# Optimization experiments

Measured on AMD Instinct MI355X. Metric: run time of the kernel, lower is better.

Reference implementation:

```python
import jax, jax.numpy as jnp
import numpy as np

N = 100_000   # nodes
E = 1_600_000 # edges (avg degree 16)
D = 64        # in_dim == hidden_dim


def setup_inputs() -> dict:
    key = jax.random.key(0)
    ks = jax.random.split(key, 9)
    scale = 1.0 / np.sqrt(D)
    x = jax.random.normal(ks[0], (N, D), jnp.float32)
    edge_index = jax.random.randint(ks[1], (2, E), 0, N, dtype=jnp.int32)
    W0 = jax.random.normal(ks[2], (D, D), jnp.float32) * scale
    b0 = jnp.zeros((D,), jnp.float32)
    W1 = jax.random.normal(ks[3], (D, D), jnp.float32) * scale
    b1 = jnp.zeros((D,), jnp.float32)
    W2 = jax.random.normal(ks[4], (D, D), jnp.float32) * scale
    b2 = jnp.zeros((D,), jnp.float32)
    return {"x": x, "edge_index": edge_index, "W0": W0, "b0": b0,
            "W1": W1, "b1": b1, "W2": W2, "b2": b2}


def _gcn_layer(h, W, b, src, dst, norm):
    # h: [N, D]; src/dst: [E+N] (self-loops included); norm: [E+N]
    h = h @ W                                  # dense transform [N, D]
    msg = h[src] * norm[:, None]               # gather + scale  [E+N, D]
    out = jax.ops.segment_sum(msg, dst, num_segments=N)  # scatter-add [N, D]
    return out + b


def reference(x, edge_index, W0, b0, W1, b1, W2, b2):
    loops = jnp.arange(N, dtype=edge_index.dtype)
    src = jnp.concatenate([edge_index[0], loops])  # [E+N]
    dst = jnp.concatenate([edge_index[1], loops])  # [E+N]
    # symmetric GCN normalization with self-loops (PyG gcn_norm)
    deg = jax.ops.segment_sum(jnp.ones_like(dst, dtype=x.dtype), dst, num_segments=N)
    d_inv = jnp.where(deg > 0, jax.lax.rsqrt(deg), 0.0)
    norm = d_inv[src] * d_inv[dst]                 # [E+N]
    for W, b in ((W0, b0), (W1, b1), (W2, b2)):
        x = jax.nn.relu(_gcn_layer(x, W, b, src, dst, norm))
    return x
```

## Files before the change

kernel.cpp:

```cpp
#include <hip/hip_runtime.h>
#include <hip/hip_fp16.h>


#define THREADS 256
#define BSH     9
#define BNODES  512
#define BCAP    9216
#define BPAD    16
#define CHUNK   4096

#if defined(__has_builtin)
#if __has_builtin(__builtin_amdgcn_fdot2) && __has_builtin(__builtin_amdgcn_perm)
#define USE_DOT2 1
#endif
#endif

typedef __attribute__((ext_vector_type(2))) _Float16 h2v;
typedef __attribute__((ext_vector_type(8))) _Float16 f16x8;
typedef __attribute__((ext_vector_type(4))) float    f32x4;

__global__ __launch_bounds__(THREADS)
void bin_kernel(const int* __restrict__ src, const int* __restrict__ dst,
                int* __restrict__ bcur, int* __restrict__ sbuf, int E) {
    __shared__ int cntb[THREADS];
    __shared__ int lstart[THREADS];
    __shared__ int gbase[THREADS];
    __shared__ int lcur[THREADS];
    __shared__ int tmp[THREADS];
    __shared__ int stagep[CHUNK];
    __shared__ unsigned char stageb[CHUNK];
    int tid = threadIdx.x;
    int e0  = blockIdx.x * CHUNK;
    int cnt = min(CHUNK, E - e0);
    int dreg[16];
#pragma unroll
    for (int j = 0; j < 16; ++j) {
        int i = tid + j * THREADS;
        dreg[j] = (i < cnt) ? dst[e0 + i] : -1;
    }
    cntb[tid] = 0;
    __syncthreads();
#pragma unroll
    for (int j = 0; j < 16; ++j)
        if (dreg[j] >= 0) atomicAdd(&cntb[dreg[j] >> BSH], 1);
    __syncthreads();
    int v = cntb[tid];
    tmp[tid] = v;
    __syncthreads();
    for (int off = 1; off < THREADS; off <<= 1) {
        int t = (tid >= off) ? tmp[tid - off] : 0;
        __syncthreads();
        tmp[tid] += t;
        __syncthreads();
    }
    lstart[tid] = tmp[tid] - v;
    lcur[tid]   = 0;
    if (v > 0) gbase[tid] = atomicAdd(&bcur[tid * BPAD], v);
    __syncthreads();
#pragma unroll
    for (int j = 0; j < 16; ++j) {
        int i = tid + j * THREADS;
        if (i < cnt) {
            int s = src[e0 + i];
            int d = dreg[j];
            int b = d >> BSH;
            int pos = atomicAdd(&lcur[b], 1);
            int idx = lstart[b] + pos;
            stagep[idx] = (s << BSH) | (d & (BNODES - 1));
            stageb[idx] = (unsigned char)b;
        }
    }
    __syncthreads();
    for (int i = tid; i < cnt; i += THREADS) {
        int b = stageb[i];
        sbuf[(size_t)b * BCAP + gbase[b] + (i - lstart[b])] = stagep[i];
    }
}

__global__ __launch_bounds__(THREADS)
void bscan_kernel(const int* __restrict__ bcur, int* __restrict__ bbase,
                  int NB, int* __restrict__ rowptr, int N, int E) {
    __shared__ int tmp[THREADS];
    int tid = threadIdx.x;
    int c = (tid < NB) ? min(bcur[tid * BPAD], BCAP) : 0;
    tmp[tid] = c;
    __syncthreads();
    for (int off = 1; off < THREADS; off <<= 1) {
        int t = (tid >= off) ? tmp[tid - off] : 0;
        __syncthreads();
        tmp[tid] += t;
        __syncthreads();
    }
    if (tid < NB) bbase[tid] = tmp[tid] - c;
    if (tid == 0) rowptr[N] = E;
}

__global__ __launch_bounds__(THREADS)
void finalize_kernel(const int* __restrict__ sbuf, const int* __restrict__ bcur,
                     const int* __restrict__ bbase, int* __restrict__ rowptr,
                     float* __restrict__ dinv, int* __restrict__ csrc, int N) {
    __shared__ int lcnt[BNODES];
    __shared__ int lexcl[BNODES];
    __shared__ int lcur[BNODES];
    __shared__ int tmp[THREADS];
    int b   = blockIdx.x;
    int tid = threadIdx.x;
    int cnt = min(bcur[b * BPAD], BCAP);
    int gb  = bbase[b];
    const int* sb = sbuf + (size_t)b * BCAP;
    for (int i = tid; i < BNODES; i += THREADS) { lcnt[i] = 0; lcur[i] = 0; }
    __syncthreads();
    for (int e = tid; e < cnt; e += THREADS)
        atomicAdd(&lcnt[sb[e] & (BNODES - 1)], 1);
    __syncthreads();
    int a0 = lcnt[2 * tid], a1 = lcnt[2 * tid + 1];
    int s  = a0 + a1;
    tmp[tid] = s;
    __syncthreads();
    for (int off = 1; off < THREADS; off <<= 1) {
        int t = (tid >= off) ? tmp[tid - off] : 0;
        __syncthreads();
        tmp[tid] += t;
        __syncthreads();
    }
    int ex = tmp[tid] - s;
    lexcl[2 * tid]     = ex;
    lexcl[2 * tid + 1] = ex + a0;
    int node = (b << BSH) + 2 * tid;
    if (node < N) {
        rowptr[node] = gb + ex;
        dinv[node]   = rsqrtf((float)(a0 + 1));
    }
    if (node + 1 < N) {
        rowptr[node + 1] = gb + ex + a0;
        dinv[node + 1]   = rsqrtf((float)(a1 + 1));
    }
    __syncthreads();
    for (int e = tid; e < cnt; e += THREADS) {
        int vv  = sb[e];
        int d   = vv & (BNODES - 1);
        int pos = atomicAdd(&lcur[d], 1);
        csrc[gb + lexcl[d] + pos] = vv >> BSH;
    }
}

__global__ __launch_bounds__(THREADS)
void gemm64_kernel(const float* __restrict__ X, __half* __restrict__ H,
                   const float* __restrict__ W, const float* __restrict__ dinv,
                   int n) {
    int lane = threadIdx.x & 63;
    int qk   = lane >> 4;
    int l16  = lane & 15;
    f16x8 bf[4][2];
#pragma unroll
    for (int t = 0; t < 4; ++t)
#pragma unroll
        for (int h = 0; h < 2; ++h) {
            const float* wp = W + (size_t)(32 * h + qk * 8) * 64 + 16 * t + l16;
#pragma unroll
            for (int j = 0; j < 8; ++j)
                bf[t][h][j] = (_Float16)wp[j * 64];
        }
    int wave  = (blockIdx.x * blockDim.x + threadIdx.x) >> 6;
    int nw    = (gridDim.x * blockDim.x) >> 6;
    int ntile = (n + 15) >> 4;
    for (int tile = wave; tile < ntile; tile += nw) {
        int rbase = tile << 4;
        int arow  = rbase + l16;
        if (arow >= n) arow = n - 1;
        const float4* xp = (const float4*)(X + (size_t)arow * 64 + qk * 8);
        float4 a0 = xp[0], a1 = xp[1];
        float4 a2 = xp[8], a3 = xp[9];
        f16x8 A0, A1;
        A0[0] = (_Float16)a0.x; A0[1] = (_Float16)a0.y;
        A0[2] = (_Float16)a0.z; A0[3] = (_Float16)a0.w;
        A0[4] = (_Float16)a1.x; A0[5] = (_Float16)a1.y;
        A0[6] = (_Float16)a1.z; A0[7] = (_Float16)a1.w;
        A1[0] = (_Float16)a2.x; A1[1] = (_Float16)a2.y;
        A1[2] = (_Float16)a2.z; A1[3] = (_Float16)a2.w;
        A1[4] = (_Float16)a3.x; A1[5] = (_Float16)a3.y;
        A1[6] = (_Float16)a3.z; A1[7] = (_Float16)a3.w;
        f32x4 acc[4];
#pragma unroll
        for (int t = 0; t < 4; ++t) {
            acc[t] = (f32x4){0.f, 0.f, 0.f, 0.f};
            acc[t] = __builtin_amdgcn_mfma_f32_16x16x32_f16(A0, bf[t][0], acc[t], 0, 0, 0);
            acc[t] = __builtin_amdgcn_mfma_f32_16x16x32_f16(A1, bf[t][1], acc[t], 0, 0, 0);
        }
        float dv[4];
#pragma unroll
        for (int r = 0; r < 4; ++r) {
            int row = rbase + qk * 4 + r;
            dv[r] = (row < n) ? dinv[row] : 0.f;
        }
#pragma unroll
        for (int r = 0; r < 4; ++r) {
            int row = rbase + qk * 4 + r;
            if (row < n) {
                __half* hp = H + (size_t)row * 64 + l16;
#pragma unroll
                for (int t = 0; t < 4; ++t)
                    hp[16 * t] = __float2half(acc[t][r] * dv[r]);
            }
        }
    }
}

__global__ __launch_bounds__(THREADS)
void agg_kernel(const __half* __restrict__ H, float* __restrict__ Y,
                const int* __restrict__ rowptr, const int* __restrict__ csrc,
                const float* __restrict__ dinv, const float* __restrict__ bias,
                int n) {
    int lane = threadIdx.x & 63;
    int grp  = lane >> 3;
    int sub  = lane & 7;
    int fl   = sub * 8;
    const int4* H4 = (const int4*)H;
    int wave = (blockIdx.x * blockDim.x + threadIdx.x) >> 6;
    int nw   = (gridDim.x * blockDim.x) >> 6;
    float4 bv0 = *(const float4*)(bias + fl);
    float4 bv1 = *(const float4*)(bias + fl + 4);
    for (int i = wave; i < n; i += nw) {
        int k0 = rowptr[i], k1 = rowptr[i + 1];
        float accf[8] = {0.f, 0.f, 0.f, 0.f, 0.f, 0.f, 0.f, 0.f};
        if (grp == 0) {
            int4 hv = H4[(size_t)i * 8 + sub];
            const __half2* hh = (const __half2*)&hv;
#pragma unroll
            for (int j = 0; j < 4; ++j) {
                float2 f = __half22float2(hh[j]);
                accf[2 * j]     += f.x;
                accf[2 * j + 1] += f.y;
            }
        }
        for (int basek = k0; basek < k1; basek += 16) {
            int kA = basek + grp, kB = kA + 8;
            bool vA = kA < k1, vB = kB < k1;
            int sA = vA ? csrc[kA] : 0;
            int sB = vB ? csrc[kB] : 0;
            int4 hA = H4[(size_t)sA * 8 + sub];
            int4 hB = H4[(size_t)sB * 8 + sub];
#ifdef USE_DOT2
            unsigned mb = (vA ? 0x3C00u : 0u) | (vB ? 0x3C000000u : 0u);
            h2v m2 = __builtin_bit_cast(h2v, mb);
            const unsigned* pa = (const unsigned*)&hA;
            const unsigned* pb = (const unsigned*)&hB;
#pragma unroll
            for (int j = 0; j < 4; ++j) {
                unsigned p0 = __builtin_amdgcn_perm(pb[j], pa[j], 0x05040100);
                unsigned p1 = __builtin_amdgcn_perm(pb[j], pa[j], 0x07060302);
                accf[2 * j]     = __builtin_amdgcn_fdot2(
                    __builtin_bit_cast(h2v, p0), m2, accf[2 * j], false);
                accf[2 * j + 1] = __builtin_amdgcn_fdot2(
                    __builtin_bit_cast(h2v, p1), m2, accf[2 * j + 1], false);
            }
#else
            float mA = vA ? 1.f : 0.f, mB = vB ? 1.f : 0.f;
            const __half2* ha = (const __half2*)&hA;
            const __half2* hb = (const __half2*)&hB;
#pragma unroll
            for (int j = 0; j < 4; ++j) {
                float2 fa = __half22float2(ha[j]);
                float2 fb = __half22float2(hb[j]);
                accf[2 * j]     = fmaf(fa.x, mA, accf[2 * j]);
                accf[2 * j]     = fmaf(fb.x, mB, accf[2 * j]);
                accf[2 * j + 1] = fmaf(fa.y, mA, accf[2 * j + 1]);
                accf[2 * j + 1] = fmaf(fb.y, mB, accf[2 * j + 1]);
            }
#endif
        }
#pragma unroll
        for (int j = 0; j < 8; ++j) {
            float a = accf[j];
            a += __shfl_xor(a, 8);
            a += __shfl_xor(a, 16);
            a += __shfl_xor(a, 32);
            accf[j] = a;
        }
        if (grp == 0) {
            float di = dinv[i];
            float4 o0, o1;
            o0.x = fmaxf(fmaf(accf[0], di, bv0.x), 0.f);
            o0.y = fmaxf(fmaf(accf[1], di, bv0.y), 0.f);
            o0.z = fmaxf(fmaf(accf[2], di, bv0.z), 0.f);
            o0.w = fmaxf(fmaf(accf[3], di, bv0.w), 0.f);
            o1.x = fmaxf(fmaf(accf[4], di, bv1.x), 0.f);
            o1.y = fmaxf(fmaf(accf[5], di, bv1.y), 0.f);
            o1.z = fmaxf(fmaf(accf[6], di, bv1.z), 0.f);
            o1.w = fmaxf(fmaf(accf[7], di, bv1.w), 0.f);
            *(float4*)(Y + (size_t)i * 64 + fl)     = o0;
            *(float4*)(Y + (size_t)i * 64 + fl + 4) = o1;
        }
    }
}

extern "C" void kernel_launch(void* const* d_in, const int* in_sizes, int n_in,
                              void* d_out, int out_size, void* d_ws, size_t ws_size,
                              hipStream_t stream) {
    const float* x  = (const float*)d_in[0];
    const int*   ei = (const int*)d_in[1];
    const float* W0 = (const float*)d_in[2];
    const float* b0 = (const float*)d_in[3];
    const float* W1 = (const float*)d_in[4];
    const float* b1 = (const float*)d_in[5];
    const float* W2 = (const float*)d_in[6];
    const float* b2 = (const float*)d_in[7];

    const int N = in_sizes[0] / 64;
    const int E = in_sizes[1] / 2;
    const int* src = ei;
    const int* dst = ei + E;
    const int NB = (N + BNODES - 1) >> BSH;

    char*  ws  = (char*)d_ws;
    size_t off = 0;
    auto alloc = [&](size_t bytes) -> void* {
        void* p = ws + off;
        off += (bytes + 255) & ~(size_t)255;
        return p;
    };
    int*    rowptr = (int*)   alloc((size_t)(N + 1) * 4);
    float*  dinv   = (float*) alloc((size_t)N * 4);
    int*    csrc   = (int*)   alloc((size_t)E * 4);
    int*    bcur   = (int*)   alloc((size_t)NB * BPAD * 4);
    int*    bbase  = (int*)   alloc((size_t)NB * 4);
    float*  actA   = (float*) alloc((size_t)N * 64 * 4);
    __half* hbuf   = (__half*)alloc((size_t)N * 64 * 2);
    int*    sbuf   = (int*)actA;
    float*  outb   = (float*)d_out;

    hipMemsetAsync(bcur, 0, (size_t)NB * BPAD * 4, stream);

    const int ngrid = 2048;
    const int ggrid = 1024;
    const int bgrid = (E + CHUNK - 1) / CHUNK;

    bin_kernel     <<<bgrid, THREADS, 0, stream>>>(src, dst, bcur, sbuf, E);
    bscan_kernel   <<<1,     THREADS, 0, stream>>>(bcur, bbase, NB, rowptr, N, E);
    finalize_kernel<<<NB,    THREADS, 0, stream>>>(sbuf, bcur, bbase, rowptr,
                                                   dinv, csrc, N);

    gemm64_kernel<<<ggrid, THREADS, 0, stream>>>(x, hbuf, W0, dinv, N);
    agg_kernel   <<<ngrid, THREADS, 0, stream>>>(hbuf, actA, rowptr, csrc, dinv, b0, N);
    gemm64_kernel<<<ggrid, THREADS, 0, stream>>>(actA, hbuf, W1, dinv, N);
    agg_kernel   <<<ngrid, THREADS, 0, stream>>>(hbuf, outb, rowptr, csrc, dinv, b1, N);
    gemm64_kernel<<<ggrid, THREADS, 0, stream>>>(outb, hbuf, W2, dinv, N);
    agg_kernel   <<<ngrid, THREADS, 0, stream>>>(hbuf, outb, rowptr, csrc, dinv, b2, N);
}
```

Measured before the change: 201.9 us.

## Process two nodes per wave in aggregation with prefetched row bounds

The aggregation kernel now splits each 64-lane wave into two 32-lane halves, each handling its own destination node. Each half loads four neighbor rows per iteration instead of two per 8-lane group, and the cross-lane reduction drops one shuffle stage. The next node's rowptr bounds are prefetched before the current node is processed, to hide that load latency. The intent is less lane idling for average degree around 17, which under-fills a 16-edge step per wave, in exchange for slightly more complex indexing. The GEMM epilogue also moves the dinv load inside the row guard.

Result: faster. 185.2 us (-8.2%).

```diff
diff --git a/kernel.cpp b/kernel.cpp
--- a/kernel.cpp
+++ b/kernel.cpp
@@ -187,23 +187,50 @@
             acc[t] = __builtin_amdgcn_mfma_f32_16x16x32_f16(A0, bf[t][0], acc[t], 0, 0, 0);
             acc[t] = __builtin_amdgcn_mfma_f32_16x16x32_f16(A1, bf[t][1], acc[t], 0, 0, 0);
         }
-        float dv[4];
-#pragma unroll
-        for (int r = 0; r < 4; ++r) {
-            int row = rbase + qk * 4 + r;
-            dv[r] = (row < n) ? dinv[row] : 0.f;
-        }
 #pragma unroll
         for (int r = 0; r < 4; ++r) {
             int row = rbase + qk * 4 + r;
             if (row < n) {
+                float dv = dinv[row];
                 __half* hp = H + (size_t)row * 64 + l16;
 #pragma unroll
                 for (int t = 0; t < 4; ++t)
-                    hp[16 * t] = __float2half(acc[t][r] * dv[r]);
+                    hp[16 * t] = __float2half(acc[t][r] * dv);
             }
         }
     }
+}
+
+__device__ __forceinline__ void pairdot(const int4& hA, const int4& hB,
+                                        bool vA, bool vB, float* accf) {
+#ifdef USE_DOT2
+    unsigned mb = (vA ? 0x3C00u : 0u) | (vB ? 0x3C000000u : 0u);
+    h2v m2 = __builtin_bit_cast(h2v, mb);
+    const unsigned* pa = (const unsigned*)&hA;
+    const unsigned* pb = (const unsigned*)&hB;
+#pragma unroll
+    for (int j = 0; j < 4; ++j) {
+        unsigned p0 = __builtin_amdgcn_perm(pb[j], pa[j], 0x05040100);
+        unsigned p1 = __builtin_amdgcn_perm(pb[j], pa[j], 0x07060302);
+        accf[2 * j]     = __builtin_amdgcn_fdot2(
+            __builtin_bit_cast(h2v, p0), m2, accf[2 * j], false);
+        accf[2 * j + 1] = __builtin_amdgcn_fdot2(
+            __builtin_bit_cast(h2v, p1), m2, accf[2 * j + 1], false);
+    }
+#else
+    float mA = vA ? 1.f : 0.f, mB = vB ? 1.f : 0.f;
+    const __half2* ha = (const __half2*)&hA;
+    const __half2* hb = (const __half2*)&hB;
+#pragma unroll
+    for (int j = 0; j < 4; ++j) {
+        float2 fa = __half22float2(ha[j]);
+        float2 fb = __half22float2(hb[j]);
+        accf[2 * j]     = fmaf(fa.x, mA, accf[2 * j]);
+        accf[2 * j]     = fmaf(fb.x, mB, accf[2 * j]);
+        accf[2 * j + 1] = fmaf(fa.y, mA, accf[2 * j + 1]);
+        accf[2 * j + 1] = fmaf(fb.y, mB, accf[2 * j + 1]);
+    }
+#endif
 }
 
 __global__ __launch_bounds__(THREADS)
@@ -212,73 +239,67 @@
                 const float* __restrict__ dinv, const float* __restrict__ bias,
                 int n) {
     int lane = threadIdx.x & 63;
-    int grp  = lane >> 3;
+    int half = lane >> 5;
+    int hl   = lane & 31;
+    int grp  = hl >> 3;
     int sub  = lane & 7;
     int fl   = sub * 8;
     const int4* H4 = (const int4*)H;
     int wave = (blockIdx.x * blockDim.x + threadIdx.x) >> 6;
     int nw   = (gridDim.x * blockDim.x) >> 6;
+    int np   = (n + 1) >> 1;
     float4 bv0 = *(const float4*)(bias + fl);
     float4 bv1 = *(const float4*)(bias + fl + 4);
-    for (int i = wave; i < n; i += nw) {
-        int k0 = rowptr[i], k1 = rowptr[i + 1];
+    int wp = wave;
+    if (wp >= np) return;
+    int node = min(2 * wp + half, n - 1);
+    int k0 = rowptr[node], k1 = rowptr[node + 1];
+    while (true) {
+        int wpn = wp + nw;
+        int noden = 0, k0n = 0, k1n = 0;
+        bool more = wpn < np;
+        if (more) {
+            noden = min(2 * wpn + half, n - 1);
+            k0n = rowptr[noden];
+            k1n = rowptr[noden + 1];
+        }
         float accf[8] = {0.f, 0.f, 0.f, 0.f, 0.f, 0.f, 0.f, 0.f};
-        if (grp == 0) {
-            int4 hv = H4[(size_t)i * 8 + sub];
-            const __half2* hh = (const __half2*)&hv;
-#pragma unroll
-            for (int j = 0; j < 4; ++j) {
-                float2 f = __half22float2(hh[j]);
-                accf[2 * j]     += f.x;
-                accf[2 * j + 1] += f.y;
+        {
+            int4 hv = H4[(size_t)node * 8 + sub];
+            if (grp == 0) {
+                const __half2* hh = (const __half2*)&hv;
+#pragma unroll
+                for (int j = 0; j < 4; ++j) {
+                    float2 f = __half22float2(hh[j]);
+                    accf[2 * j]     += f.x;
+                    accf[2 * j + 1] += f.y;
+                }
             }
         }
         for (int basek = k0; basek < k1; basek += 16) {
-            int kA = basek + grp, kB = kA + 8;
-            bool vA = kA < k1, vB = kB < k1;
-            int sA = vA ? csrc[kA] : 0;
-            int sB = vB ? csrc[kB] : 0;
-            int4 hA = H4[(size_t)sA * 8 + sub];
-            int4 hB = H4[(size_t)sB * 8 + sub];
-#ifdef USE_DOT2
-            unsigned mb = (vA ? 0x3C00u : 0u) | (vB ? 0x3C000000u : 0u);
-            h2v m2 = __builtin_bit_cast(h2v, mb);
-            const unsigned* pa = (const unsigned*)&hA;
-            const unsigned* pb = (const unsigned*)&hB;
-#pragma unroll
-            for (int j = 0; j < 4; ++j) {
-                unsigned p0 = __builtin_amdgcn_perm(pb[j], pa[j], 0x05040100);
-                unsigned p1 = __builtin_amdgcn_perm(pb[j], pa[j], 0x07060302);
-                accf[2 * j]     = __builtin_amdgcn_fdot2(
-                    __builtin_bit_cast(h2v, p0), m2, accf[2 * j], false);
-                accf[2 * j + 1] = __builtin_amdgcn_fdot2(
-                    __builtin_bit_cast(h2v, p1), m2, accf[2 * j + 1], false);
-            }
-#else
-            float mA = vA ? 1.f : 0.f, mB = vB ? 1.f : 0.f;
-            const __half2* ha = (const __half2*)&hA;
-            const __half2* hb = (const __half2*)&hB;
-#pragma unroll
-            for (int j = 0; j < 4; ++j) {
-                float2 fa = __half22float2(ha[j]);
-                float2 fb = __half22float2(hb[j]);
-                accf[2 * j]     = fmaf(fa.x, mA, accf[2 * j]);
-                accf[2 * j]     = fmaf(fb.x, mB, accf[2 * j]);
-                accf[2 * j + 1] = fmaf(fa.y, mA, accf[2 * j + 1]);
-                accf[2 * j + 1] = fmaf(fb.y, mB, accf[2 * j + 1]);
-            }
-#endif
+            int  kk0 = basek + grp;
+            int  kk1 = kk0 + 4, kk2 = kk0 + 8, kk3 = kk0 + 12;
+            bool v0 = kk0 < k1, v1 = kk1 < k1, v2 = kk2 < k1, v3 = kk3 < k1;
+            int  s0 = v0 ? csrc[kk0] : 0;
+            int  s1 = v1 ? csrc[kk1] : 0;
+            int  s2 = v2 ? csrc[kk2] : 0;
+            int  s3 = v3 ? csrc[kk3] : 0;
+            int4 h0 = H4[(size_t)s0 * 8 + sub];
+            int4 h1 = H4[(size_t)s1 * 8 + sub];
+            int4 h2 = H4[(size_t)s2 * 8 + sub];
+            int4 h3 = H4[(size_t)s3 * 8 + sub];
+            pairdot(h0, h1, v0, v1, accf);
+            pairdot(h2, h3, v2, v3, accf);
         }
 #pragma unroll
         for (int j = 0; j < 8; ++j) {
             float a = accf[j];
             a += __shfl_xor(a, 8);
             a += __shfl_xor(a, 16);
-            a += __shfl_xor(a, 32);
             accf[j] = a;
         }
-        if (grp == 0) {
-            float di = dinv[i];
+        if (grp == 0 && 2 * wp + half < n) {
+            float di = dinv[node];
             float4 o0, o1;
             o0.x = fmaxf(fmaf(accf[0], di, bv0.x), 0.f);
             o0.y = fmaxf(fmaf(accf[1], di, bv0.y), 0.f);
@@ -288,9 +309,11 @@
             o1.y = fmaxf(fmaf(accf[5], di, bv1.y), 0.f);
             o1.z = fmaxf(fmaf(accf[6], di, bv1.z), 0.f);
             o1.w = fmaxf(fmaf(accf[7], di, bv1.w), 0.f);
-            *(float4*)(Y + (size_t)i * 64 + fl)     = o0;
-            *(float4*)(Y + (size_t)i * 64 + fl + 4) = o1;
-        }
+            *(float4*)(Y + (size_t)node * 64 + fl)     = o0;
+            *(float4*)(Y + (size_t)node * 64 + fl + 4) = o1;
+        }
+        if (!more) break;
+        wp = wpn; node = noden; k0 = k0n; k1 = k1n;
     }
 }
 
```
